# Optimization experiments

Measured on AMD Instinct MI355X. Metric: run time of the kernel, lower is better.

The kernel has to match this reference:

```python
import jax, jax.numpy as jnp
import numpy as np

N = 1024          # total nodes (includes BATCH virtual roots, processed first)
BATCH = 8         # number of trees / images
IN_DIM = 2048     # inputs_dim
EMBED = 200       # embed_dim ('start' token at row 0)
HID = 1024        # hidden_dim
NUM_CLASSES = 151 # len(classes), class 0 = background (never committed)
X_DIM = IN_DIM + EMBED


def setup_inputs() -> dict:
    key = jax.random.key(0)
    ks = jax.random.split(key, 8)
    # topologically-ordered tree: node i's parent is some j < i; first BATCH nodes are roots
    rng = np.random.RandomState(0)
    parent = np.full(N, -1, dtype=np.int64)
    for i in range(BATCH, N):
        parent[i] = rng.randint(0, i)
    sx = 1.0 / np.sqrt(X_DIM)
    sh = 1.0 / np.sqrt(HID)
    return dict(
        features=jax.random.normal(ks[0], (N, IN_DIM), jnp.float32),
        parent_idx=jnp.asarray(parent),
        batch_size=BATCH,
        W_px=jax.random.normal(ks[1], (X_DIM, HID), jnp.float32) * sx,
        b_px=jnp.zeros((HID,), jnp.float32),
        W_iofux=jax.random.normal(ks[2], (X_DIM, 5 * HID), jnp.float32) * sx,
        b_iofux=jnp.zeros((5 * HID,), jnp.float32),
        W_iofuh=jax.random.normal(ks[3], (HID, 5 * HID), jnp.float32) * sh,
        b_iofuh=jnp.zeros((5 * HID,), jnp.float32),
        W_out=jax.random.normal(ks[4], (HID, NUM_CLASSES), jnp.float32) * sh,
        b_out=jnp.zeros((NUM_CLASSES,), jnp.float32),
        embed_table=jax.random.normal(ks[5], (NUM_CLASSES + 1, EMBED), jnp.float32),
    )


def reference(features, parent_idx, batch_size, W_px, b_px, W_iofux, b_iofux,
              W_iofuh, b_iofuh, W_out, b_out, embed_table):
    n = features.shape[0]
    hid = W_iofuh.shape[0]

    def step(carry, i):
        h_all, c_all, commit_all = carry
        p = parent_idx[i]
        root = p < 0
        ps = jnp.maximum(p, 0)
        gate = jnp.where(root, 0.0, 1.0)
        ph = h_all[ps] * gate          # parent hidden (zeros at root)
        pc = c_all[ps] * gate          # parent cell   (zeros at root)
        # parent's committed label embedding; row 0 = 'start' token for roots
        pe = embed_table[jnp.where(root, 0, commit_all[ps])]
        x = jnp.concatenate([features[i], pe])          # [X_DIM]
        proj_x = x @ W_px + b_px                        # highway projection
        g = x @ W_iofux + b_iofux + ph @ W_iofuh + b_iofuh  # [5*HID]
        ig, og, fg, ug, rg = jnp.split(g, 5)
        ig = jax.nn.sigmoid(ig)
        og = jax.nn.sigmoid(og)
        fg = jax.nn.sigmoid(fg)
        rg = jax.nn.sigmoid(rg)
        ug = jnp.tanh(ug)
        c = ig * ug + fg * pc
        h = og * jnp.tanh(c)
        h_final = rg * h + (1.0 - rg) * proj_x          # highway output
        dist = h_final @ W_out + b_out                  # class logits
        # greedy commitment, background (class 0) excluded
        commit = (jnp.argmax(dist[1:]) + 1).astype(jnp.int32)
        carry = (h_all.at[i].set(h_final),
                 c_all.at[i].set(c),
                 commit_all.at[i].set(commit))
        return carry, dist

    init = (jnp.zeros((n, hid), features.dtype),
            jnp.zeros((n, hid), features.dtype),
            jnp.zeros((n,), jnp.int32))
    (h_all, c_all, commit_all), dists = jax.lax.scan(step, init, jnp.arange(n))
    # order puts the batch_size virtual roots last; they are then dropped
    out_dists = dists[batch_size:]
    out_commitments = jnp.concatenate(
        [commit_all[batch_size:], jnp.zeros((batch_size,), jnp.int32)])
    return out_dists, out_commitments
```

## Files before the change

kernel.cpp:

```cpp
#include <hip/hip_runtime.h>
#include <math.h>


#define NBLK 512
#define NTHR 512
#define OUT_COMMIT_OFF (1016 * 151)

typedef short bf16x8 __attribute__((ext_vector_type(8)));
typedef float f32x16 __attribute__((ext_vector_type(16)));

__device__ __align__(16) short g_Wih_hi[160 * 128 * 32 * 8 + 512];
__device__ __align__(16) short g_Wih_lo[160 * 128 * 32 * 8 + 512];
__device__ __align__(16) short g_Wpre_hi[192 * 256 * 32 * 8 + 512];
__device__ __align__(16) short g_Wpre_lo[192 * 256 * 32 * 8 + 512];
__device__ __align__(16) short g_fpk_hi[32 * 256 * 32 * 8 + 512];
__device__ __align__(16) short g_fpk_lo[32 * 256 * 32 * 8 + 512];
__device__ __align__(16) unsigned g_Apk_hi[128 * 128 * 32 * 4 + 256];
__device__ __align__(16) unsigned g_Apk_lo[128 * 128 * 32 * 4 + 256];
__device__ __align__(16) unsigned g_Spk_hi[128 * 128 * 32 * 4 + 256];
__device__ __align__(16) unsigned g_Spk_lo[128 * 128 * 32 * 4 + 256];
__device__ __align__(16) short g_Wout_hi[5 * 128 * 32 * 8 + 512];
__device__ __align__(16) short g_Wout_lo[5 * 128 * 32 * 8 + 512];

__device__ __align__(16) float g_c[1024 * 1024];
__device__ __align__(16) float g_pre[1024 * 6144];
__device__ __align__(16) float g_gate[1120 * 5120];
__device__ __align__(16) float g_embG[152 * 6144];
__device__ __align__(16) float g_embpad[162 * 224];
__device__ __align__(16) float g_zero[128];
__device__ __align__(16) unsigned long long g_pamax[128 * 32 * 5 + 64];
__device__ int g_lvl_start[1025];
__device__ int g_tile_off[1025];
__device__ int g_order[1024];
__device__ int g_prow[1024];
__device__ int g_cstart[1025];
__device__ int g_clist[1024];
__device__ int g_numlvl;
__device__ unsigned g_barcnt[512];

__device__ __forceinline__ unsigned short bf16_rn(float x) {
  union { float f; unsigned u; } v; v.f = x;
  unsigned r = v.u + 0x7fffu + ((v.u >> 16) & 1u);
  return (unsigned short)(r >> 16);
}
__device__ __forceinline__ float bf16_tof(unsigned short h) {
  union { float f; unsigned u; } v; v.u = ((unsigned)h) << 16; return v.f;
}
__device__ __forceinline__ void split2(float x, unsigned short& hi, unsigned short& lo) {
  hi = bf16_rn(x);
  lo = bf16_rn(x - bf16_tof(hi));
}
__device__ __forceinline__ f32x16 mfma3(bf16x8 ah, bf16x8 al, bf16x8 bh, bf16x8 bl, f32x16 c) {
  c = __builtin_amdgcn_mfma_f32_32x32x16_bf16(ah, bh, c, 0, 0, 0);
  c = __builtin_amdgcn_mfma_f32_32x32x16_bf16(ah, bl, c, 0, 0, 0);
  c = __builtin_amdgcn_mfma_f32_32x32x16_bf16(al, bh, c, 0, 0, 0);
  return c;
}

#define AST_F(p, v)  __hip_atomic_store((p), (v), __ATOMIC_RELAXED, __HIP_MEMORY_SCOPE_AGENT)
#define AST_U(p, v)  __hip_atomic_store((p), (v), __ATOMIC_RELAXED, __HIP_MEMORY_SCOPE_AGENT)

#define LD8(p, o) (*(const bf16x8*)((p) + (o)))

template<int NS>
__device__ __forceinline__ f32x16 gemm1x(const short* __restrict__ pah,
                                         const short* __restrict__ pal,
                                         const short* __restrict__ pbh,
                                         const short* __restrict__ pbl) {
  f32x16 acc = {};
  bf16x8 ahe = LD8(pah, 0),   ale = LD8(pal, 0);
  bf16x8 bhe = LD8(pbh, 0),   ble = LD8(pbl, 0);
  bf16x8 aho = LD8(pah, 512), alo = LD8(pal, 512);
  bf16x8 bho = LD8(pbh, 512), blo = LD8(pbl, 512);
  for (int g = 0; g + 1 < NS / 2; ++g) {
    const size_t o = (size_t)(2 * g + 2) * 512;
    acc = mfma3(ahe, ale, bhe, ble, acc);
    ahe = LD8(pah, o); ale = LD8(pal, o); bhe = LD8(pbh, o); ble = LD8(pbl, o);
    acc = mfma3(aho, alo, bho, blo, acc);
    aho = LD8(pah, o + 512); alo = LD8(pal, o + 512);
    bho = LD8(pbh, o + 512); blo = LD8(pbl, o + 512);
  }
  acc = mfma3(ahe, ale, bhe, ble, acc);
  acc = mfma3(aho, alo, bho, blo, acc);
  return acc;
}

template<int NS>
__device__ __forceinline__ void gemm2x(const short* __restrict__ pa0h, const short* __restrict__ pa0l,
                                       const short* __restrict__ pa1h, const short* __restrict__ pa1l,
                                       const short* __restrict__ pbh,  const short* __restrict__ pbl,
                                       f32x16& acc0, f32x16& acc1) {
  bf16x8 a0he = LD8(pa0h, 0),   a0le = LD8(pa0l, 0);
  bf16x8 a1he = LD8(pa1h, 0),   a1le = LD8(pa1l, 0);
  bf16x8 bhe  = LD8(pbh, 0),    ble  = LD8(pbl, 0);
  bf16x8 a0ho = LD8(pa0h, 512), a0lo = LD8(pa0l, 512);
  bf16x8 a1ho = LD8(pa1h, 512), a1lo = LD8(pa1l, 512);
  bf16x8 bho  = LD8(pbh, 512),  blo  = LD8(pbl, 512);
  for (int g = 0; g + 1 < NS / 2; ++g) {
    const size_t o = (size_t)(2 * g + 2) * 512;
    acc0 = mfma3(a0he, a0le, bhe, ble, acc0);
    acc1 = mfma3(a1he, a1le, bhe, ble, acc1);
    a0he = LD8(pa0h, o); a0le = LD8(pa0l, o);
    a1he = LD8(pa1h, o); a1le = LD8(pa1l, o);
    bhe = LD8(pbh, o);   ble = LD8(pbl, o);
    acc0 = mfma3(a0ho, a0lo, bho, blo, acc0);
    acc1 = mfma3(a1ho, a1lo, bho, blo, acc1);
    a0ho = LD8(pa0h, o + 512); a0lo = LD8(pa0l, o + 512);
    a1ho = LD8(pa1h, o + 512); a1lo = LD8(pa1l, o + 512);
    bho = LD8(pbh, o + 512);   blo = LD8(pbl, o + 512);
  }
  acc0 = mfma3(a0he, a0le, bhe, ble, acc0);
  acc1 = mfma3(a1he, a1le, bhe, ble, acc1);
  acc0 = mfma3(a0ho, a0lo, bho, blo, acc0);
  acc1 = mfma3(a1ho, a1lo, bho, blo, acc1);
}

__device__ __forceinline__ void gload_lds16(const float* g, float* s) {
  __builtin_amdgcn_global_load_lds(
      (const __attribute__((address_space(1))) void*)g,
      (__attribute__((address_space(3))) void*)s, 16, 0, 0);
}

__device__ __forceinline__ void gbar(unsigned int* gen) {
  __syncthreads();
  if (threadIdx.x == 0) {
    ++(*gen);
    __hip_atomic_fetch_add(&g_barcnt[((unsigned)blockIdx.x & 15) << 5], 1u,
                           __ATOMIC_RELAXED, __HIP_MEMORY_SCOPE_AGENT);
    const unsigned int target = (unsigned int)NBLK * (*gen);
    for (;;) {
      unsigned int s = 0;
      #pragma unroll
      for (int i = 0; i < 16; ++i)
        s += __hip_atomic_load(&g_barcnt[i << 5], __ATOMIC_RELAXED, __HIP_MEMORY_SCOPE_AGENT);
      if (s >= target) break;
      __builtin_amdgcn_s_sleep(1);
    }
  }
  __syncthreads();
}

__device__ __forceinline__ int pamax_combine(int prow) {
  float bv = -3.4e38f; int bi = 1;
  #pragma unroll
  for (int nt = 0; nt < 5; ++nt) {
    const unsigned long long pu = g_pamax[prow * 5 + nt];
    const float v = __uint_as_float((unsigned)pu);
    if (v > bv) { bv = v; bi = (int)(pu >> 32); }
  }
  return bi;
}

__global__ void prep_kernel(const int* __restrict__ parent,
                            const float* __restrict__ emb,
                            float* __restrict__ out) {
  __shared__ int lvl[1024];
  __shared__ int cnt[1024];
  __shared__ int c2[1024];
  __shared__ int changed;
  const int i = threadIdx.x;
  const int p = parent[i];
  lvl[i] = (p < 0) ? 0 : -1;
  for (;;) {
    if (i == 0) changed = 0;
    __syncthreads();
    if (lvl[i] < 0 && lvl[p] >= 0) { lvl[i] = lvl[p] + 1; changed = 1; }
    __syncthreads();
    const int ch = changed;
    __syncthreads();
    if (ch == 0) break;
  }
  cnt[i] = 0;
  __syncthreads();
  atomicAdd(&cnt[lvl[i]], 1);
  __syncthreads();
  if (i == 0) {
    int acc = 0, nl = 0, ta = 0;
    for (int l2 = 0; l2 < 1024; ++l2) {
      g_lvl_start[l2] = acc;
      g_tile_off[l2] = ta;
      if (cnt[l2] > 0) nl = l2 + 1;
      acc += cnt[l2];
      ta += (cnt[l2] + 31) >> 5;
    }
    g_lvl_start[1024] = acc;
    g_tile_off[1024] = ta;
    g_numlvl = nl;
  }
  __syncthreads();
  cnt[i] = 0;
  __syncthreads();
  {
    const int ni = atomicAdd(&cnt[lvl[i]], 1);
    g_order[g_lvl_start[lvl[i]] + ni] = i;
    g_prow[i] = ((g_tile_off[lvl[i]] + (ni >> 5)) << 5) | (ni & 31);
  }
  __syncthreads();
  cnt[i] = 0;
  __syncthreads();
  if (p >= 0) atomicAdd(&cnt[p], 1);
  __syncthreads();
  if (i == 0) {
    int a2 = 0;
    for (int n2 = 0; n2 < 1024; ++n2) { g_cstart[n2] = a2; a2 += cnt[n2]; }
    g_cstart[1024] = a2;
  }
  __syncthreads();
  c2[i] = 0;
  __syncthreads();
  if (p >= 0) {
    const int q = g_cstart[p] + atomicAdd(&c2[p], 1);
    g_clist[q] = i;
  }
  for (int j = i; j < 162 * 224; j += 1024) {
    const int r = j / 224, cc = j - r * 224;
    g_embpad[j] = (r < 152 && cc < 200) ? emb[r * 200 + cc] : 0.0f;
  }
  __syncthreads();
  {
    const int n0 = g_tile_off[1] * 16384;
    for (int e = i; e < n0; e += 1024) { g_Apk_hi[e] = 0u; g_Apk_lo[e] = 0u; }
  }
  if (i < 512) g_barcnt[i] = 0u;
  if (i < 128) g_zero[i] = 0.0f;
  if (i < 8) out[OUT_COMMIT_OFF + 1016 + i] = 0.0f;
}

#define U_WIH  (160 * 128 * 32)
#define U_WPRE (192 * 256 * 32)
#define U_FEAT (32 * 256 * 32)
#define U_WOUT (5 * 128 * 32)
__global__ void pack_all(const float* __restrict__ Wpx, const float* __restrict__ Wix,
                         const float* __restrict__ Wih, const float* __restrict__ feat,
                         const float* __restrict__ Wout) {
  const int tot = U_WIH + U_WPRE + U_FEAT + U_WOUT;
  for (int u = blockIdx.x * blockDim.x + threadIdx.x; u < tot; u += gridDim.x * blockDim.x) {
    if (u < U_WIH) {
      const int j = u & 31, kb = (u >> 5) & 127, nt = u >> 12;
      const int n = nt * 32 + j;
      #pragma unroll
      for (int kk = 0; kk < 8; ++kk) {
        unsigned short h, l;
        split2(Wih[(size_t)(kb * 8 + kk) * 5120 + n], h, l);
        g_Wih_hi[(size_t)u * 8 + kk] = (short)h;
        g_Wih_lo[(size_t)u * 8 + kk] = (short)l;
      }
    } else if (u < U_WIH + U_WPRE) {
      const int u2 = u - U_WIH;
      const int j = u2 & 31, kb = (u2 >> 5) & 255, nt = u2 >> 13;
      const int n = nt * 32 + j;
      #pragma unroll
      for (int kk = 0; kk < 8; ++kk) {
        const int k = kb * 8 + kk;
        const float v = (n < 1024) ? Wpx[(size_t)k * 1024 + n]
                                   : Wix[(size_t)k * 5120 + (n - 1024)];
        unsigned short h, l; split2(v, h, l);
        g_Wpre_hi[(size_t)u2 * 8 + kk] = (short)h;
        g_Wpre_lo[(size_t)u2 * 8 + kk] = (short)l;
      }
    } else if (u < U_WIH + U_WPRE + U_FEAT) {
      const int u3 = u - U_WIH - U_WPRE;
      const int j = u3 & 31, kb = (u3 >> 5) & 255, mt = u3 >> 13;
      const int m = mt * 32 + j;
      #pragma unroll
      for (int kk = 0; kk < 8; ++kk) {
        unsigned short h, l;
        split2(feat[(size_t)m * 2048 + kb * 8 + kk], h, l);
        g_fpk_hi[(size_t)u3 * 8 + kk] = (short)h;
        g_fpk_lo[(size_t)u3 * 8 + kk] = (short)l;
      }
    } else {
      const int u4 = u - U_WIH - U_WPRE - U_FEAT;
      const int j = u4 & 31, kb = (u4 >> 5) & 127, nt = u4 >> 12;
      const int col = nt * 32 + j;
      #pragma unroll
      for (int kk = 0; kk < 8; ++kk) {
        const float v = (col < 151) ? Wout[(size_t)(kb * 8 + kk) * 151 + col] : 0.f;
        unsigned short h, l; split2(v, h, l);
        g_Wout_hi[(size_t)u4 * 8 + kk] = (short)h;
        g_Wout_lo[(size_t)u4 * 8 + kk] = (short)l;
      }
    }
  }
}

#define STEP(ACC, AV)                                  \
  ACC.x += AV.x * b0.x; ACC.y += AV.x * b0.y;          \
  ACC.x += AV.y * b1.x; ACC.y += AV.y * b1.y;          \
  ACC.x += AV.z * b2.x; ACC.y += AV.z * b2.y;          \
  ACC.x += AV.w * b3.x; ACC.y += AV.w * b3.y;

__device__ __forceinline__ void chunk_fma64(const float* __restrict__ Ab,
                                            const float* __restrict__ Bb,
                                            int l, float2* acc) {
  #pragma unroll
  for (int kq = 0; kq < 16; ++kq) {
    const float4 a0 = *(const float4*)(Ab + 0 * 64 + (kq << 2));
    const float4 a1 = *(const float4*)(Ab + 1 * 64 + (kq << 2));
    const float4 a2 = *(const float4*)(Ab + 2 * 64 + (kq << 2));
    const float4 a3 = *(const float4*)(Ab + 3 * 64 + (kq << 2));
    const float2 b0 = *(const float2*)(Bb + ((kq << 2) + 0) * 128 + (l << 1));
    const float2 b1 = *(const float2*)(Bb + ((kq << 2) + 1) * 128 + (l << 1));
    const float2 b2 = *(const float2*)(Bb + ((kq << 2) + 2) * 128 + (l << 1));
    const float2 b3 = *(const float2*)(Bb + ((kq << 2) + 3) * 128 + (l << 1));
    STEP(acc[0], a0) STEP(acc[1], a1) STEP(acc[2], a2) STEP(acc[3], a3)
  }
}

__global__ __launch_bounds__(512, 2) void emb_gemm(
    const float* __restrict__ Wpx, const float* __restrict__ Wix,
    const float* __restrict__ bpx, const float* __restrict__ bix,
    const float* __restrict__ bih) {
  __shared__ __align__(16) float smem[20480];
  const int tid = threadIdx.x, w = tid >> 6, l = tid & 63;
  const int mt = blockIdx.x / 48, ct = blockIdx.x % 48;
  const int c0 = ct << 7;
  const bool isproj = ct < 8;
  const float* W1 = isproj ? Wpx : Wix;
  const size_t N1 = isproj ? 1024 : 5120;
  const int c0x = isproj ? c0 : c0 - 1024;
  const int arow = (mt << 5) + (w << 2) + (l >> 4);
  const float* asrc = g_embpad + arow * 224 + ((l & 15) << 2);
  const int brow = (w << 3) + (l >> 5);
  const int bcol = (l & 31) << 2;

  auto STAGE = [&](int c, int buf) {
    float* base = smem + buf * 10240;
    const int kb = c << 6;
    gload_lds16(asrc + kb, base + (w << 8));
    #pragma unroll
    for (int j = 0; j < 4; ++j) {
      const int k = kb + brow + (j << 1);
      const float* srcB = (k < 200) ? (W1 + (size_t)(2048 + k) * N1 + c0x + bcol)
                                    : (g_zero + bcol);
      gload_lds16(srcB, base + 2048 + (((w << 3) + (j << 1)) << 7));
    }
  };

  float2 acc[4] = {{0.f,0.f},{0.f,0.f},{0.f,0.f},{0.f,0.f}};
  STAGE(0, 0);
  asm volatile("s_waitcnt vmcnt(0)" ::: "memory");
  __builtin_amdgcn_s_barrier();
  for (int c = 0; c < 4; ++c) {
    if (c + 1 < 4) STAGE(c + 1, (c + 1) & 1);
    const int cur = c & 1;
    chunk_fma64(smem + cur * 10240 + (w << 8), smem + cur * 10240 + 2048, l, acc);
    asm volatile("s_waitcnt vmcnt(0) lgkmcnt(0)" ::: "memory");
    __builtin_amdgcn_s_barrier();
  }
  const int cc = c0 + (l << 1);
  float2 bias;
  if (isproj) { bias.x = bpx[cc]; bias.y = bpx[cc + 1]; }
  else { bias.x = bix[cc - 1024] + bih[cc - 1024]; bias.y = bix[cc - 1023] + bih[cc - 1023]; }
  #pragma unroll
  for (int i = 0; i < 4; ++i) {
    const int r = (mt << 5) + (w << 2) + i;
    if (r < 152) {
      float2 o = { acc[i].x + bias.x, acc[i].y + bias.y };
      *(float2*)(g_embG + (size_t)r * 6144 + cc) = o;
    }
  }
}

__global__ __launch_bounds__(256, 2) void pre_gemm_mfma() {
  const int tid = threadIdx.x, w = tid >> 6, l = tid & 63;
  const int bid = (int)blockIdx.x;
  const int x = bid & 7, e = bid >> 3;
  const int ct = x + ((e % 6) << 3);
  const int mt = e / 6;
  const int lk = l >> 5, lj = l & 31;
  const size_t abase0 = ((size_t)((2 * mt) * 256 + lk) * 32 + lj) * 8;
  const size_t abase1 = abase0 + 65536;
  const int nt = ct * 4 + w;
  const size_t bbase = ((size_t)(nt * 256 + lk) * 32 + lj) * 8;
  f32x16 acc0 = {}, acc1 = {};
  gemm2x<128>(g_fpk_hi + abase0, g_fpk_lo + abase0,
              g_fpk_hi + abase1, g_fpk_lo + abase1,
              g_Wpre_hi + bbase, g_Wpre_lo + bbase, acc0, acc1);
  const int colg = ct * 128 + w * 32 + lj;
  const int rb = mt * 64 + 4 * lk;
  #pragma unroll
  for (int reg = 0; reg < 16; ++reg) {
    const int r = rb + (reg & 3) + 8 * (reg >> 2);
    g_pre[(size_t)r * 6144 + colg] = acc0[reg];
    g_pre[(size_t)(r + 32) * 6144 + colg] = acc1[reg];
  }
}

__device__ void dist_tile(int Lp, int mt, int nt, const float* __restrict__ bout,
                          float* __restrict__ out, int tid, int w, int l,
                          int lk, int lj, float* smem, float* sdist) {
  const int s0p = g_lvl_start[Lp];
  const int Mp = g_lvl_start[Lp + 1] - s0p;
  const int tg = g_tile_off[Lp] + mt;
  const size_t ab = (size_t)tg * 32768 + (size_t)w * 4096 + (size_t)((lk << 5) + lj) * 8;
  const size_t bb = (size_t)nt * 32768 + (size_t)w * 4096 + (size_t)((lk << 5) + lj) * 8;
  f32x16 part = gemm1x<8>((const short*)g_Spk_hi + ab, (const short*)g_Spk_lo + ab,
                          g_Wout_hi + bb, g_Wout_lo + bb);
  #pragma unroll
  for (int e = 0; e < 16; ++e) smem[((e << 3) + w) * 64 + l] = part[e];
  __syncthreads();
  const int e0 = tid >> 6, lr = tid & 63;
  #pragma unroll
  for (int h = 0; h < 2; ++h) {
    const int e = e0 + (h << 3);
    float v = 0.f;
    #pragma unroll
    for (int ww = 0; ww < 8; ++ww) v += smem[((e << 3) + ww) * 64 + lr];
    const int row = (e & 3) + ((e >> 2) << 3) + ((lr >> 5) << 2);
    const int cl = lr & 31;
    const int col = (nt << 5) + cl;
    float vb = -3.4e38f;
    if (col < 151) {
      vb = v + bout[col];
      const int m = (mt << 5) + row;
      if (m < Mp) {
        const int node = g_order[s0p + m];
        if (node >= 8) out[(size_t)(node - 8) * 151 + col] = vb;
      }
    }
    sdist[row * 33 + cl] = (col >= 151 || col == 0) ? -3.4e38f : vb;
  }
  __syncthreads();
  if (tid < 32) {
    const int m = (mt << 5) + tid;
    if (m < Mp) {
      float bv = -3.4e38f; int bi = 1;
      for (int cl = 0; cl < 32; ++cl) {
        const float v = sdist[tid * 33 + cl];
        if (v > bv) { bv = v; bi = (nt << 5) + cl; }
      }
      const unsigned long long pu =
          ((unsigned long long)(unsigned)bi << 32) | (unsigned long long)__float_as_uint(bv);
      AST_U(&g_pamax[(tg * 32 + tid) * 5 + nt], pu);
    }
  }
  __syncthreads();
}

__global__ __launch_bounds__(NTHR, 2) void lstm_main(
    const int* __restrict__ parent,
    const float* __restrict__ bout,
    float* __restrict__ out) {
  __shared__ float smem[8192];
  __shared__ float sdist[1056];
  unsigned int gen = 0;
  const int tid = threadIdx.x;
  const int bid = (int)blockIdx.x;
  const int w = tid >> 6, l = tid & 63;
  const int lk = l >> 5, lj = l & 31;
  const int nl = g_numlvl;
  const int x = bid & 7;
  const int u2 = 63 - (bid >> 3);

  for (int L = 0; L < nl; ++L) {
    const int s0 = g_lvl_start[L];
    const int M  = g_lvl_start[L + 1] - s0;
    const int nmt = (M + 31) >> 5;
    const int toffL = g_tile_off[L];
    const int s0p = (L > 0) ? g_lvl_start[L - 1] : 0;
    const int Mp = (L > 0) ? (s0 - s0p) : 0;
    const int nmtp = (Mp + 31) >> 5;
    const int D = nmtp * 5;

    if (L > 0 && bid < D) {
      dist_tile(L - 1, bid / 5, bid % 5, bout, out, tid, w, l, lk, lj, smem, sdist);
    }
    {
      const int TPX = nmt * 20;
      for (int t = u2; t < TPX; t += 64) {
        const int mt = t / 20, ci = t - (t / 20) * 20;
        const int ct = x + (ci << 3);
        const int tg = toffL + mt;
        const size_t ab = (size_t)tg * 32768 + (size_t)w * 4096 + (size_t)((lk << 5) + lj) * 8;
        const size_t bb = (size_t)ct * 32768 + (size_t)w * 4096 + (size_t)((lk << 5) + lj) * 8;
        f32x16 part = gemm1x<8>((const short*)g_Apk_hi + ab, (const short*)g_Apk_lo + ab,
                                g_Wih_hi + bb, g_Wih_lo + bb);
        #pragma unroll
        for (int e = 0; e < 16; ++e) smem[((e << 3) + w) * 64 + l] = part[e];
        __syncthreads();
        const int e0 = tid >> 6, lr = tid & 63;
        #pragma unroll
        for (int h = 0; h < 2; ++h) {
          const int e = e0 + (h << 3);
          float v = 0.f;
          #pragma unroll
          for (int ww = 0; ww < 8; ++ww) v += smem[((e << 3) + ww) * 64 + lr];
          const int row = (e & 3) + ((e >> 2) << 3) + ((lr >> 5) << 2);
          const int m = (mt << 5) + row;
          if (m < M) {
            const int col = (ct << 5) + (lr & 31);
            AST_F(&g_gate[(size_t)(s0 + m) * 5120 + col], v);
          }
        }
        __syncthreads();
      }
    }
    gbar(&gen);

    if (L > 0) {
      for (int ni2 = bid; ni2 < Mp; ni2 += NBLK) {
        const int pn = g_order[s0p + ni2];
        if (pn >= 8 && tid == 0)
          out[OUT_COMMIT_OFF + pn - 8] = (float)pamax_combine(g_prow[pn]);
      }
    }
    for (int ni = bid; ni < M; ni += NBLK) {
      const int node = g_order[s0 + ni];
      const int p = parent[node];
      const int er = (p < 0) ? 0 : pamax_combine(g_prow[p]);
      const float* gt = g_gate + (size_t)(s0 + ni) * 5120;
      const float* pre = g_pre + (size_t)node * 6144;
      const float* eg  = g_embG + (size_t)er * 6144;
      const int prow = g_prow[node];
      const size_t sbase = (size_t)(prow >> 5) * 16384 + (size_t)(prow & 31) * 4;
      const int cs = g_cstart[node], ce = g_cstart[node + 1];
      const int j = tid << 1;
      const float2 g0 = *(const float2*)(gt + j);
      const float2 g1 = *(const float2*)(gt + 1024 + j);
      const float2 g2 = *(const float2*)(gt + 2048 + j);
      const float2 g3 = *(const float2*)(gt + 3072 + j);
      const float2 g4 = *(const float2*)(gt + 4096 + j);
      const float2 p0 = *(const float2*)(pre + j);
      const float2 p1 = *(const float2*)(pre + 1024 + j);
      const float2 p2 = *(const float2*)(pre + 2048 + j);
      const float2 p3 = *(const float2*)(pre + 3072 + j);
      const float2 p4 = *(const float2*)(pre + 4096 + j);
      const float2 p5 = *(const float2*)(pre + 5120 + j);
      const float2 e0v = *(const float2*)(eg + j);
      const float2 e1 = *(const float2*)(eg + 1024 + j);
      const float2 e2 = *(const float2*)(eg + 2048 + j);
      const float2 e3 = *(const float2*)(eg + 3072 + j);
      const float2 e4 = *(const float2*)(eg + 4096 + j);
      const float2 e5 = *(const float2*)(eg + 5120 + j);
      float2 pc2 = {0.f, 0.f};
      if (p >= 0) pc2 = *(const float2*)(g_c + (size_t)p * 1024 + j);

      float cv[2], hf[2];
      #pragma unroll
      for (int e = 0; e < 2; ++e) {
        const float proj = ((e == 0) ? p0.x : p0.y) + ((e == 0) ? e0v.x : e0v.y);
        const float vi = ((e == 0) ? g0.x : g0.y) + ((e == 0) ? p1.x : p1.y) + ((e == 0) ? e1.x : e1.y);
        const float vo = ((e == 0) ? g1.x : g1.y) + ((e == 0) ? p2.x : p2.y) + ((e == 0) ? e2.x : e2.y);
        const float vf = ((e == 0) ? g2.x : g2.y) + ((e == 0) ? p3.x : p3.y) + ((e == 0) ? e3.x : e3.y);
        const float vu = ((e == 0) ? g3.x : g3.y) + ((e == 0) ? p4.x : p4.y) + ((e == 0) ? e4.x : e4.y);
        const float vr = ((e == 0) ? g4.x : g4.y) + ((e == 0) ? p5.x : p5.y) + ((e == 0) ? e5.x : e5.y);
        const float ig = 1.f / (1.f + expf(-vi));
        const float og = 1.f / (1.f + expf(-vo));
        const float fg = 1.f / (1.f + expf(-vf));
        const float rg = 1.f / (1.f + expf(-vr));
        const float ug = tanhf(vu);
        const float pc = (e == 0) ? pc2.x : pc2.y;
        const float c = ig * ug + fg * pc;
        const float h = og * tanhf(c);
        cv[e] = c;
        hf[e] = rg * h + (1.f - rg) * proj;
      }
      AST_F(&g_c[(size_t)node * 1024 + j], cv[0]);
      AST_F(&g_c[(size_t)node * 1024 + j + 1], cv[1]);
      unsigned short h0, l0, h1, l1;
      split2(hf[0], h0, l0);
      split2(hf[1], h1, l1);
      const unsigned hpk = (unsigned)h0 | ((unsigned)h1 << 16);
      const unsigned lpk = (unsigned)l0 | ((unsigned)l1 << 16);
      const size_t soff = sbase + (size_t)(j >> 3) * 128 + ((j & 7) >> 1);
      AST_U(&g_Spk_hi[soff], hpk);
      AST_U(&g_Spk_lo[soff], lpk);
      for (int ci = cs; ci < ce; ++ci) {
        const int prc = g_prow[g_clist[ci]];
        const size_t aoff = (size_t)(prc >> 5) * 16384 + (size_t)(j >> 3) * 128
                          + (size_t)(prc & 31) * 4 + ((j & 7) >> 1);
        AST_U(&g_Apk_hi[aoff], hpk);
        AST_U(&g_Apk_lo[aoff], lpk);
      }
    }
    gbar(&gen);
  }

  {
    const int Lf = nl - 1;
    const int s0f = g_lvl_start[Lf];
    const int Mf = g_lvl_start[Lf + 1] - s0f;
    const int nmtf = (Mf + 31) >> 5;
    const int Df = nmtf * 5;
    if (bid < Df) {
      dist_tile(Lf, bid / 5, bid % 5, bout, out, tid, w, l, lk, lj, smem, sdist);
    }
    gbar(&gen);
    for (int ni = bid; ni < Mf; ni += NBLK) {
      const int pn = g_order[s0f + ni];
      if (pn >= 8 && tid == 0)
        out[OUT_COMMIT_OFF + pn - 8] = (float)pamax_combine(g_prow[pn]);
    }
  }
}

extern "C" void kernel_launch(void* const* d_in, const int* in_sizes, int n_in,
                              void* d_out, int out_size, void* d_ws, size_t ws_size,
                              hipStream_t stream) {
  const float* feat   = (const float*)d_in[0];
  const int*   parent = (const int*)d_in[1];
  const float* Wpx  = (const float*)d_in[3];
  const float* bpx  = (const float*)d_in[4];
  const float* Wix  = (const float*)d_in[5];
  const float* bix  = (const float*)d_in[6];
  const float* Wih  = (const float*)d_in[7];
  const float* bih  = (const float*)d_in[8];
  const float* Wout = (const float*)d_in[9];
  const float* bout = (const float*)d_in[10];
  const float* emb  = (const float*)d_in[11];
  float* out = (float*)d_out;

  hipLaunchKernelGGL(prep_kernel, dim3(1), dim3(1024), 0, stream, parent, emb, out);
  hipLaunchKernelGGL(pack_all, dim3(2048), dim3(256), 0, stream, Wpx, Wix, Wih, feat, Wout);
  hipLaunchKernelGGL(emb_gemm, dim3(240), dim3(512), 0, stream, Wpx, Wix, bpx, bix, bih);
  hipLaunchKernelGGL(pre_gemm_mfma, dim3(768), dim3(256), 0, stream);
  hipLaunchKernelGGL(lstm_main, dim3(NBLK), dim3(NTHR), 0, stream,
                     parent, bout, out);
}
```

Before: 623.7 us.

## Merge weight packing and embedding GEMM into one prologue kernel; relax atomic stores

Fuses the pack_all weight/feature bf16 split-packing and the emb_gemm embedding GEMM into a single prologue1 launch. Blocks 0-239 run the embedding GEMM and the remaining 784 blocks do the packing, with the packing order changed so Wpre and features come first. This removes one kernel launch and lets the two independent jobs overlap on the device. Separately, the atomic stores used for cross-block communication become plain stores, with explicit agent-scope release and acquire fences added around the grid barrier. The fences are meant to keep visibility correct, but they add cost to every barrier, and plain stores could reorder if any path relied on the old atomics outside gbar.

```diff
diff --git a/kernel.cpp b/kernel.cpp
--- a/kernel.cpp
+++ b/kernel.cpp
@@ -57,8 +57,8 @@
   return c;
 }
 
-#define AST_F(p, v)  __hip_atomic_store((p), (v), __ATOMIC_RELAXED, __HIP_MEMORY_SCOPE_AGENT)
-#define AST_U(p, v)  __hip_atomic_store((p), (v), __ATOMIC_RELAXED, __HIP_MEMORY_SCOPE_AGENT)
+#define AST_F(p, v)  (*(p) = (v))
+#define AST_U(p, v)  (*(p) = (v))
 
 #define LD8(p, o) (*(const bf16x8*)((p) + (o)))
 
@@ -125,6 +125,7 @@
   __syncthreads();
   if (threadIdx.x == 0) {
     ++(*gen);
+    __builtin_amdgcn_fence(__ATOMIC_RELEASE, "agent");
     __hip_atomic_fetch_add(&g_barcnt[((unsigned)blockIdx.x & 15) << 5], 1u,
                            __ATOMIC_RELAXED, __HIP_MEMORY_SCOPE_AGENT);
     const unsigned int target = (unsigned int)NBLK * (*gen);
@@ -136,6 +137,7 @@
       if (s >= target) break;
       __builtin_amdgcn_s_sleep(1);
     }
+    __builtin_amdgcn_fence(__ATOMIC_ACQUIRE, "agent");
   }
   __syncthreads();
 }
@@ -226,63 +228,10 @@
   if (i < 8) out[OUT_COMMIT_OFF + 1016 + i] = 0.0f;
 }
 
-#define U_WIH  (160 * 128 * 32)
 #define U_WPRE (192 * 256 * 32)
 #define U_FEAT (32 * 256 * 32)
+#define U_WIH  (160 * 128 * 32)
 #define U_WOUT (5 * 128 * 32)
-__global__ void pack_all(const float* __restrict__ Wpx, const float* __restrict__ Wix,
-                         const float* __restrict__ Wih, const float* __restrict__ feat,
-                         const float* __restrict__ Wout) {
-  const int tot = U_WIH + U_WPRE + U_FEAT + U_WOUT;
-  for (int u = blockIdx.x * blockDim.x + threadIdx.x; u < tot; u += gridDim.x * blockDim.x) {
-    if (u < U_WIH) {
-      const int j = u & 31, kb = (u >> 5) & 127, nt = u >> 12;
-      const int n = nt * 32 + j;
-      #pragma unroll
-      for (int kk = 0; kk < 8; ++kk) {
-        unsigned short h, l;
-        split2(Wih[(size_t)(kb * 8 + kk) * 5120 + n], h, l);
-        g_Wih_hi[(size_t)u * 8 + kk] = (short)h;
-        g_Wih_lo[(size_t)u * 8 + kk] = (short)l;
-      }
-    } else if (u < U_WIH + U_WPRE) {
-      const int u2 = u - U_WIH;
-      const int j = u2 & 31, kb = (u2 >> 5) & 255, nt = u2 >> 13;
-      const int n = nt * 32 + j;
-      #pragma unroll
-      for (int kk = 0; kk < 8; ++kk) {
-        const int k = kb * 8 + kk;
-        const float v = (n < 1024) ? Wpx[(size_t)k * 1024 + n]
-                                   : Wix[(size_t)k * 5120 + (n - 1024)];
-        unsigned short h, l; split2(v, h, l);
-        g_Wpre_hi[(size_t)u2 * 8 + kk] = (short)h;
-        g_Wpre_lo[(size_t)u2 * 8 + kk] = (short)l;
-      }
-    } else if (u < U_WIH + U_WPRE + U_FEAT) {
-      const int u3 = u - U_WIH - U_WPRE;
-      const int j = u3 & 31, kb = (u3 >> 5) & 255, mt = u3 >> 13;
-      const int m = mt * 32 + j;
-      #pragma unroll
-      for (int kk = 0; kk < 8; ++kk) {
-        unsigned short h, l;
-        split2(feat[(size_t)m * 2048 + kb * 8 + kk], h, l);
-        g_fpk_hi[(size_t)u3 * 8 + kk] = (short)h;
-        g_fpk_lo[(size_t)u3 * 8 + kk] = (short)l;
-      }
-    } else {
-      const int u4 = u - U_WIH - U_WPRE - U_FEAT;
-      const int j = u4 & 31, kb = (u4 >> 5) & 127, nt = u4 >> 12;
-      const int col = nt * 32 + j;
-      #pragma unroll
-      for (int kk = 0; kk < 8; ++kk) {
-        const float v = (col < 151) ? Wout[(size_t)(kb * 8 + kk) * 151 + col] : 0.f;
-        unsigned short h, l; split2(v, h, l);
-        g_Wout_hi[(size_t)u4 * 8 + kk] = (short)h;
-        g_Wout_lo[(size_t)u4 * 8 + kk] = (short)l;
-      }
-    }
-  }
-}
 
 #define STEP(ACC, AV)                                  \
   ACC.x += AV.x * b0.x; ACC.y += AV.x * b0.y;          \
@@ -307,57 +256,112 @@
   }
 }
 
-__global__ __launch_bounds__(512, 2) void emb_gemm(
+__global__ __launch_bounds__(512, 2) void prologue1(
     const float* __restrict__ Wpx, const float* __restrict__ Wix,
     const float* __restrict__ bpx, const float* __restrict__ bix,
-    const float* __restrict__ bih) {
+    const float* __restrict__ bih, const float* __restrict__ Wih,
+    const float* __restrict__ Wout, const float* __restrict__ feat) {
   __shared__ __align__(16) float smem[20480];
-  const int tid = threadIdx.x, w = tid >> 6, l = tid & 63;
-  const int mt = blockIdx.x / 48, ct = blockIdx.x % 48;
-  const int c0 = ct << 7;
-  const bool isproj = ct < 8;
-  const float* W1 = isproj ? Wpx : Wix;
-  const size_t N1 = isproj ? 1024 : 5120;
-  const int c0x = isproj ? c0 : c0 - 1024;
-  const int arow = (mt << 5) + (w << 2) + (l >> 4);
-  const float* asrc = g_embpad + arow * 224 + ((l & 15) << 2);
-  const int brow = (w << 3) + (l >> 5);
-  const int bcol = (l & 31) << 2;
-
-  auto STAGE = [&](int c, int buf) {
-    float* base = smem + buf * 10240;
-    const int kb = c << 6;
-    gload_lds16(asrc + kb, base + (w << 8));
+  const int bid = (int)blockIdx.x, tid = threadIdx.x;
+  const int l = tid & 63;
+  if (bid < 240) {
+    const int w = tid >> 6;
+    const int mt = bid / 48, ct = bid % 48;
+    const int c0 = ct << 7;
+    const bool isproj = ct < 8;
+    const float* W1 = isproj ? Wpx : Wix;
+    const size_t N1 = isproj ? 1024 : 5120;
+    const int c0x = isproj ? c0 : c0 - 1024;
+    const int arow = (mt << 5) + (w << 2) + (l >> 4);
+    const float* asrc = g_embpad + arow * 224 + ((l & 15) << 2);
+    const int brow = (w << 3) + (l >> 5);
+    const int bcol = (l & 31) << 2;
+
+    auto STAGE = [&](int c, int buf) {
+      float* base = smem + buf * 10240;
+      const int kb = c << 6;
+      gload_lds16(asrc + kb, base + (w << 8));
+      #pragma unroll
+      for (int j = 0; j < 4; ++j) {
+        const int k = kb + brow + (j << 1);
+        const float* srcB = (k < 200) ? (W1 + (size_t)(2048 + k) * N1 + c0x + bcol)
+                                      : (g_zero + bcol);
+        gload_lds16(srcB, base + 2048 + (((w << 3) + (j << 1)) << 7));
+      }
+    };
+
+    float2 acc[4] = {{0.f,0.f},{0.f,0.f},{0.f,0.f},{0.f,0.f}};
+    STAGE(0, 0);
+    asm volatile("s_waitcnt vmcnt(0)" ::: "memory");
+    __builtin_amdgcn_s_barrier();
+    for (int c = 0; c < 4; ++c) {
+      if (c + 1 < 4) STAGE(c + 1, (c + 1) & 1);
+      const int cur = c & 1;
+      chunk_fma64(smem + cur * 10240 + (w << 8), smem + cur * 10240 + 2048, l, acc);
+      asm volatile("s_waitcnt vmcnt(0) lgkmcnt(0)" ::: "memory");
+      __builtin_amdgcn_s_barrier();
+    }
+    const int cc = c0 + (l << 1);
+    float2 bias;
+    if (isproj) { bias.x = bpx[cc]; bias.y = bpx[cc + 1]; }
+    else { bias.x = bix[cc - 1024] + bih[cc - 1024]; bias.y = bix[cc - 1023] + bih[cc - 1023]; }
     #pragma unroll
-    for (int j = 0; j < 4; ++j) {
-      const int k = kb + brow + (j << 1);
-      const float* srcB = (k < 200) ? (W1 + (size_t)(2048 + k) * N1 + c0x + bcol)
-                                    : (g_zero + bcol);
-      gload_lds16(srcB, base + 2048 + (((w << 3) + (j << 1)) << 7));
-    }
-  };
-
-  float2 acc[4] = {{0.f,0.f},{0.f,0.f},{0.f,0.f},{0.f,0.f}};
-  STAGE(0, 0);
-  asm volatile("s_waitcnt vmcnt(0)" ::: "memory");
-  __builtin_amdgcn_s_barrier();
-  for (int c = 0; c < 4; ++c) {
-    if (c + 1 < 4) STAGE(c + 1, (c + 1) & 1);
-    const int cur = c & 1;
-    chunk_fma64(smem + cur * 10240 + (w << 8), smem + cur * 10240 + 2048, l, acc);
-    asm volatile("s_waitcnt vmcnt(0) lgkmcnt(0)" ::: "memory");
-    __builtin_amdgcn_s_barrier();
-  }
-  const int cc = c0 + (l << 1);
-  float2 bias;
-  if (isproj) { bias.x = bpx[cc]; bias.y = bpx[cc + 1]; }
-  else { bias.x = bix[cc - 1024] + bih[cc - 1024]; bias.y = bix[cc - 1023] + bih[cc - 1023]; }
-  #pragma unroll
-  for (int i = 0; i < 4; ++i) {
-    const int r = (mt << 5) + (w << 2) + i;
-    if (r < 152) {
-      float2 o = { acc[i].x + bias.x, acc[i].y + bias.y };
-      *(float2*)(g_embG + (size_t)r * 6144 + cc) = o;
+    for (int i = 0; i < 4; ++i) {
+      const int r = (mt << 5) + (w << 2) + i;
+      if (r < 152) {
+        float2 o = { acc[i].x + bias.x, acc[i].y + bias.y };
+        *(float2*)(g_embG + (size_t)r * 6144 + cc) = o;
+      }
+    }
+  } else {
+    const int tot = U_WPRE + U_FEAT + U_WIH + U_WOUT;
+    for (int u = (bid - 240) * 512 + tid; u < tot; u += 784 * 512) {
+      if (u < U_WPRE) {
+        const int j = u & 31, kb = (u >> 5) & 255, nt = u >> 13;
+        const int n = nt * 32 + j;
+        #pragma unroll
+        for (int kk = 0; kk < 8; ++kk) {
+          const int k = kb * 8 + kk;
+          const float v = (n < 1024) ? Wpx[(size_t)k * 1024 + n]
+                                     : Wix[(size_t)k * 5120 + (n - 1024)];
+          unsigned short h, lo; split2(v, h, lo);
+          g_Wpre_hi[(size_t)u * 8 + kk] = (short)h;
+          g_Wpre_lo[(size_t)u * 8 + kk] = (short)lo;
+        }
+      } else if (u < U_WPRE + U_FEAT) {
+        const int u3 = u - U_WPRE;
+        const int j = u3 & 31, kb = (u3 >> 5) & 255, mt = u3 >> 13;
+        const int m = mt * 32 + j;
+        #pragma unroll
+        for (int kk = 0; kk < 8; ++kk) {
+          unsigned short h, lo;
+          split2(feat[(size_t)m * 2048 + kb * 8 + kk], h, lo);
+          g_fpk_hi[(size_t)u3 * 8 + kk] = (short)h;
+          g_fpk_lo[(size_t)u3 * 8 + kk] = (short)lo;
+        }
+      } else if (u < U_WPRE + U_FEAT + U_WIH) {
+        const int u2 = u - U_WPRE - U_FEAT;
+        const int j = u2 & 31, kb = (u2 >> 5) & 127, nt = u2 >> 12;
+        const int n = nt * 32 + j;
+        #pragma unroll
+        for (int kk = 0; kk < 8; ++kk) {
+          unsigned short h, lo;
+          split2(Wih[(size_t)(kb * 8 + kk) * 5120 + n], h, lo);
+          g_Wih_hi[(size_t)u2 * 8 + kk] = (short)h;
+          g_Wih_lo[(size_t)u2 * 8 + kk] = (short)lo;
+        }
+      } else {
+        const int u4 = u - U_WPRE - U_FEAT - U_WIH;
+        const int j = u4 & 31, kb = (u4 >> 5) & 127, nt = u4 >> 12;
+        const int col = nt * 32 + j;
+        #pragma unroll
+        for (int kk = 0; kk < 8; ++kk) {
+          const float v = (col < 151) ? Wout[(size_t)(kb * 8 + kk) * 151 + col] : 0.f;
+          unsigned short h, lo; split2(v, h, lo);
+          g_Wout_hi[(size_t)u4 * 8 + kk] = (short)h;
+          g_Wout_lo[(size_t)u4 * 8 + kk] = (short)lo;
+        }
+      }
     }
   }
 }
@@ -612,8 +616,8 @@
   float* out = (float*)d_out;
 
   hipLaunchKernelGGL(prep_kernel, dim3(1), dim3(1024), 0, stream, parent, emb, out);
-  hipLaunchKernelGGL(pack_all, dim3(2048), dim3(256), 0, stream, Wpx, Wix, Wih, feat, Wout);
-  hipLaunchKernelGGL(emb_gemm, dim3(240), dim3(512), 0, stream, Wpx, Wix, bpx, bix, bih);
+  hipLaunchKernelGGL(prologue1, dim3(1024), dim3(512), 0, stream,
+                     Wpx, Wix, bpx, bix, bih, Wih, Wout, feat);
   hipLaunchKernelGGL(pre_gemm_mfma, dim3(768), dim3(256), 0, stream);
   hipLaunchKernelGGL(lstm_main, dim3(NBLK), dim3(NTHR), 0, stream,
                      parent, bout, out);
```

Result: slower. 938.8 us (+50.5%).

## Replace static tile assignment with atomic work queue and unroll gemm prefetch

Applied to the files above, without the earlier changes.

The static strided assignment of gate GEMM tiles to blocks (u2 stride 64 within each XCD group) is replaced by a dynamic queue. Each of the 8 groups fetches tile indices from its own global atomic counter, offset per level, so blocks that finish their dist_tile work early can take more tiles. The gemm1x helper is also hand-unrolled for 8 k-steps with a four-deep register prefetch. The cost is an atomic and two extra barriers per tile, plus higher register pressure from the deeper prefetch.

```diff
diff --git a/kernel.cpp b/kernel.cpp
--- a/kernel.cpp
+++ b/kernel.cpp
@@ -37,6 +37,7 @@
 __device__ int g_clist[1024];
 __device__ int g_numlvl;
 __device__ unsigned g_barcnt[512];
+__device__ unsigned g_q[256];
 
 __device__ __forceinline__ unsigned short bf16_rn(float x) {
   union { float f; unsigned u; } v; v.f = x;
@@ -62,26 +63,27 @@
 
 #define LD8(p, o) (*(const bf16x8*)((p) + (o)))
 
-template<int NS>
-__device__ __forceinline__ f32x16 gemm1x(const short* __restrict__ pah,
-                                         const short* __restrict__ pal,
-                                         const short* __restrict__ pbh,
-                                         const short* __restrict__ pbl) {
+__device__ __forceinline__ f32x16 gemm1x8(const short* __restrict__ pah,
+                                          const short* __restrict__ pal,
+                                          const short* __restrict__ pbh,
+                                          const short* __restrict__ pbl) {
   f32x16 acc = {};
-  bf16x8 ahe = LD8(pah, 0),   ale = LD8(pal, 0);
-  bf16x8 bhe = LD8(pbh, 0),   ble = LD8(pbl, 0);
-  bf16x8 aho = LD8(pah, 512), alo = LD8(pal, 512);
-  bf16x8 bho = LD8(pbh, 512), blo = LD8(pbl, 512);
-  for (int g = 0; g + 1 < NS / 2; ++g) {
-    const size_t o = (size_t)(2 * g + 2) * 512;
-    acc = mfma3(ahe, ale, bhe, ble, acc);
-    ahe = LD8(pah, o); ale = LD8(pal, o); bhe = LD8(pbh, o); ble = LD8(pbl, o);
-    acc = mfma3(aho, alo, bho, blo, acc);
-    aho = LD8(pah, o + 512); alo = LD8(pal, o + 512);
-    bho = LD8(pbh, o + 512); blo = LD8(pbl, o + 512);
-  }
-  acc = mfma3(ahe, ale, bhe, ble, acc);
-  acc = mfma3(aho, alo, bho, blo, acc);
+  bf16x8 a0h=LD8(pah,0),    a0l=LD8(pal,0),    b0h=LD8(pbh,0),    b0l=LD8(pbl,0);
+  bf16x8 a1h=LD8(pah,512),  a1l=LD8(pal,512),  b1h=LD8(pbh,512),  b1l=LD8(pbl,512);
+  bf16x8 a2h=LD8(pah,1024), a2l=LD8(pal,1024), b2h=LD8(pbh,1024), b2l=LD8(pbl,1024);
+  bf16x8 a3h=LD8(pah,1536), a3l=LD8(pal,1536), b3h=LD8(pbh,1536), b3l=LD8(pbl,1536);
+  acc = mfma3(a0h, a0l, b0h, b0l, acc);
+  a0h=LD8(pah,2048); a0l=LD8(pal,2048); b0h=LD8(pbh,2048); b0l=LD8(pbl,2048);
+  acc = mfma3(a1h, a1l, b1h, b1l, acc);
+  a1h=LD8(pah,2560); a1l=LD8(pal,2560); b1h=LD8(pbh,2560); b1l=LD8(pbl,2560);
+  acc = mfma3(a2h, a2l, b2h, b2l, acc);
+  a2h=LD8(pah,3072); a2l=LD8(pal,3072); b2h=LD8(pbh,3072); b2l=LD8(pbl,3072);
+  acc = mfma3(a3h, a3l, b3h, b3l, acc);
+  a3h=LD8(pah,3584); a3l=LD8(pal,3584); b3h=LD8(pbh,3584); b3l=LD8(pbl,3584);
+  acc = mfma3(a0h, a0l, b0h, b0l, acc);
+  acc = mfma3(a1h, a1l, b1h, b1l, acc);
+  acc = mfma3(a2h, a2l, b2h, b2l, acc);
+  acc = mfma3(a3h, a3l, b3h, b3l, acc);
   return acc;
 }
 
@@ -222,6 +224,7 @@
     for (int e = i; e < n0; e += 1024) { g_Apk_hi[e] = 0u; g_Apk_lo[e] = 0u; }
   }
   if (i < 512) g_barcnt[i] = 0u;
+  if (i < 256) g_q[i] = 0u;
   if (i < 128) g_zero[i] = 0.0f;
   if (i < 8) out[OUT_COMMIT_OFF + 1016 + i] = 0.0f;
 }
@@ -395,8 +398,8 @@
   const int tg = g_tile_off[Lp] + mt;
   const size_t ab = (size_t)tg * 32768 + (size_t)w * 4096 + (size_t)((lk << 5) + lj) * 8;
   const size_t bb = (size_t)nt * 32768 + (size_t)w * 4096 + (size_t)((lk << 5) + lj) * 8;
-  f32x16 part = gemm1x<8>((const short*)g_Spk_hi + ab, (const short*)g_Spk_lo + ab,
-                          g_Wout_hi + bb, g_Wout_lo + bb);
+  f32x16 part = gemm1x8((const short*)g_Spk_hi + ab, (const short*)g_Spk_lo + ab,
+                        g_Wout_hi + bb, g_Wout_lo + bb);
   #pragma unroll
   for (int e = 0; e < 16; ++e) smem[((e << 3) + w) * 64 + l] = part[e];
   __syncthreads();
@@ -444,6 +447,7 @@
     float* __restrict__ out) {
   __shared__ float smem[8192];
   __shared__ float sdist[1056];
+  __shared__ unsigned s_task;
   unsigned int gen = 0;
   const int tid = threadIdx.x;
   const int bid = (int)blockIdx.x;
@@ -451,7 +455,6 @@
   const int lk = l >> 5, lj = l & 31;
   const int nl = g_numlvl;
   const int x = bid & 7;
-  const int u2 = 63 - (bid >> 3);
 
   for (int L = 0; L < nl; ++L) {
     const int s0 = g_lvl_start[L];
@@ -467,15 +470,23 @@
       dist_tile(L - 1, bid / 5, bid % 5, bout, out, tid, w, l, lk, lj, smem, sdist);
     }
     {
-      const int TPX = nmt * 20;
-      for (int t = u2; t < TPX; t += 64) {
-        const int mt = t / 20, ci = t - (t / 20) * 20;
+      const unsigned TPX = (unsigned)(nmt * 20);
+      const unsigned qbase = 20u * (unsigned)toffL + 64u * (unsigned)L;
+      for (;;) {
+        if (tid == 0)
+          s_task = __hip_atomic_fetch_add(&g_q[x << 5], 1u,
+                                          __ATOMIC_RELAXED, __HIP_MEMORY_SCOPE_AGENT) - qbase;
+        __syncthreads();
+        const unsigned t = s_task;
+        if (t >= TPX) { __syncthreads(); break; }
+        const int mt = (int)(t / 20), ci = (int)(t - (t / 20) * 20);
         const int ct = x + (ci << 3);
         const int tg = toffL + mt;
         const size_t ab = (size_t)tg * 32768 + (size_t)w * 4096 + (size_t)((lk << 5) + lj) * 8;
         const size_t bb = (size_t)ct * 32768 + (size_t)w * 4096 + (size_t)((lk << 5) + lj) * 8;
-        f32x16 part = gemm1x<8>((const short*)g_Apk_hi + ab, (const short*)g_Apk_lo + ab,
-                                g_Wih_hi + bb, g_Wih_lo + bb);
+        f32x16 part = gemm1x8((const short*)g_Apk_hi + ab, (const short*)g_Apk_lo + ab,
+                              g_Wih_hi + bb, g_Wih_lo + bb);
+        __syncthreads();
         #pragma unroll
         for (int e = 0; e < 16; ++e) smem[((e << 3) + w) * 64 + l] = part[e];
         __syncthreads();
```

After: 663.4 us. 6.4% more time.
